# Kernel optimization log

Measured on AMD Instinct MI355X. Metric: run time of the kernel, lower is better.

## Reference

```python
import jax, jax.numpy as jnp
import numpy as np

DIM = 1024
N_HEADS = 16
HEAD_DIM = DIM // N_HEADS


def setup_inputs() -> dict:
    key = jax.random.key(0)
    ks = jax.random.split(key, 5)
    s = 1.0 / np.sqrt(DIM)
    return {
        "x": jax.random.normal(ks[0], (2, 2048, DIM), dtype=jnp.float32),
        "w_qkv": jax.random.normal(ks[1], (DIM, 3 * DIM), dtype=jnp.float32) * s,
        "b_qkv": jnp.zeros((3 * DIM,), dtype=jnp.float32),
        "w_proj": jax.random.normal(ks[2], (DIM, DIM), dtype=jnp.float32) * s,
        "b_proj": jnp.zeros((DIM,), dtype=jnp.float32),
    }


def reference(x, w_qkv, b_qkv, w_proj, b_proj):
    B, T, C = x.shape
    qkv = x @ w_qkv + b_qkv                      # [B,T,3C]
    qkv = qkv.reshape(B, T, 3, N_HEADS, HEAD_DIM)
    q, k, v = qkv[:, :, 0], qkv[:, :, 1], qkv[:, :, 2]  # [B,T,H,D]
    scale = 1.0 / np.sqrt(HEAD_DIM)
    scores = jnp.einsum("bqhd,bkhd->bhqk", q, k) * scale  # [B,H,T,T]
    attn = jax.nn.softmax(scores, axis=-1)
    out = jnp.einsum("bhqk,bkhd->bqhd", attn, v)          # [B,T,H,D]
    out = out.reshape(B, T, C)
    return out @ w_proj + b_proj
```

## Files before the change

kernel.cpp:

```cpp
#include <hip/hip_runtime.h>

typedef unsigned short u16;
typedef unsigned int   u32;
typedef __bf16 bf16x8 __attribute__((ext_vector_type(8)));
typedef float  f32x4  __attribute__((ext_vector_type(4)));
typedef float  f32x16 __attribute__((ext_vector_type(16)));

#define TSEQ 2048
#define NHEAD 16
#define HDIM 64
#define CDIM 1024
#define N3   3072
#define MROWS 4096

__device__ __forceinline__ u16 f2bf(float f) {
    union { float f; u32 u; } v; v.f = f;
    u32 r = v.u + 0x7FFFu + ((v.u >> 16) & 1u);
    return (u16)(r >> 16);
}

__device__ __forceinline__ u32 pkbf(float a, float b) {
#if __has_builtin(__builtin_amdgcn_cvt_pk_bf16_f32)
    typedef __bf16 bf16x2 __attribute__((ext_vector_type(2)));
    bf16x2 t = __builtin_amdgcn_cvt_pk_bf16_f32(a, b);
    union { bf16x2 v; u32 u; } c; c.v = t; return c.u;
#else
    union { float f; u32 u; } ua, ub; ua.f = a; ub.f = b;
    u32 sel = 0x07060302, d;
    asm("v_perm_b32 %0, %1, %2, %3" : "=v"(d) : "v"(ub.u), "v"(ua.u), "v"(sel));
    return d;
#endif
}

__device__ __forceinline__ void gld16(const u16* g, u16* l) {
    __builtin_amdgcn_global_load_lds(
        (const __attribute__((address_space(1))) u32*)g,
        (__attribute__((address_space(3))) u32*)l, 16, 0, 0);
}

__global__ __launch_bounds__(256) void prep_kernel(const float* __restrict__ x,
                                                   const float* __restrict__ wqkv,
                                                   const float* __restrict__ wproj,
                                                   u16* __restrict__ Xb,
                                                   u16* __restrict__ oqkv, u16* __restrict__ oproj) {
    __shared__ float tile[32][33];
    const int bx = blockIdx.x;
    const int tid = threadIdx.x;
    if (bx < 4096) {
        int i = bx * 256 + tid;
        float4 v = reinterpret_cast<const float4*>(x)[i];
        ushort4 o;
        o.x = f2bf(v.x); o.y = f2bf(v.y); o.z = f2bf(v.z); o.w = f2bf(v.w);
        reinterpret_cast<ushort4*>(Xb)[i] = o;
        return;
    }
    int idx = bx - 4096;
    int bnx = idx & 127;
    int k0  = (idx >> 7) * 32;
    const float* in; u16* out; int N, n0;
    if (bnx < 96) { in = wqkv;  out = oqkv;  N = 3072; n0 = bnx * 32; }
    else          { in = wproj; out = oproj; N = 1024; n0 = (bnx - 96) * 32; }
    int tx = tid & 31, ty = tid >> 5;
#pragma unroll
    for (int i = 0; i < 4; i++)
        tile[ty + i * 8][tx] = in[(size_t)(k0 + ty + i * 8) * N + n0 + tx];
    __syncthreads();
#pragma unroll
    for (int i = 0; i < 4; i++)
        out[(size_t)(n0 + ty + i * 8) * 1024 + k0 + tx] = f2bf(tile[tx][ty + i * 8]);
}

__global__ __launch_bounds__(256) void gemm_qkv(const u16* __restrict__ A, const u16* __restrict__ Bt,
                                                const float* __restrict__ bias, u16* __restrict__ Qf,
                                                u16* __restrict__ Kf, u16* __restrict__ Vf) {
    __shared__ __align__(16) u16 Al[128 * 32];
    __shared__ __align__(16) u16 Bl[128 * 32];
    __shared__ __align__(16) u16 Im[16384];
    const int tid  = threadIdx.x;
    const int lane = tid & 63;
    const int wave = tid >> 6;
    const int wm = (wave >> 1) * 64;
    const int wn = (wave & 1) * 64;
    const int row0 = blockIdx.x * 128;
    const int col0 = blockIdx.y * 128;
    const int lr = lane & 15;
    const int lq = lane >> 4;
    const float c2 = 0.125f * 1.44269504088896f;

    f32x4 acc[4][4];
#pragma unroll
    for (int i = 0; i < 4; i++)
#pragma unroll
        for (int j = 0; j < 4; j++) acc[i][j] = f32x4{0.f, 0.f, 0.f, 0.f};

    const int sr = tid >> 2, sc_ = (tid & 3) * 8;

    for (int k0 = 0; k0 < CDIM; k0 += 32) {
#pragma unroll
        for (int s = 0; s < 2; s++) {
            int i = tid + s * 256;
            int r = sr + s * 64;
            gld16(&A[(size_t)(row0 + r) * CDIM + k0 + sc_], &Al[i * 8]);
            gld16(&Bt[(size_t)(col0 + r) * CDIM + k0 + sc_], &Bl[i * 8]);
        }
        __syncthreads();
        bf16x8 af[4], bfr[4];
#pragma unroll
        for (int t = 0; t < 4; t++) {
            af[t]  = *reinterpret_cast<const bf16x8*>(&Al[(wm + t * 16 + lr) * 32 + lq * 8]);
            bfr[t] = *reinterpret_cast<const bf16x8*>(&Bl[(wn + t * 16 + lr) * 32 + lq * 8]);
        }
#pragma unroll
        for (int mt = 0; mt < 4; mt++)
#pragma unroll
            for (int nt = 0; nt < 4; nt++)
                acc[mt][nt] = __builtin_amdgcn_mfma_f32_16x16x32_bf16(af[mt], bfr[nt], acc[mt][nt], 0, 0, 0);
        __syncthreads();
    }

    const int region = col0 >> 10;
    const int h_base = (col0 & 1023) >> 6;
#pragma unroll
    for (int mt = 0; mt < 4; mt++) {
#pragma unroll
        for (int nt = 0; nt < 4; nt++) {
            int n_local = wn + nt * 16 + lr;
            float bv = bias[col0 + n_local];
            int h_local = n_local >> 6;
            int d = n_local & 63;
#pragma unroll
            for (int r = 0; r < 4; r++) {
                int m_local = wm + mt * 16 + lq * 4 + r;
                float v = acc[mt][nt][r] + bv;
                if (region == 0) {
                    int qt_local = m_local >> 5, q31 = m_local & 31;
                    int kc = d >> 4, l5b = (d >> 3) & 1, j = d & 7;
                    int lc = (h_local * 4 + qt_local) * 4 + kc;
                    Im[lc * 512 + (l5b * 32 + q31) * 8 + j] = f2bf(v * c2);
                } else if (region == 1) {
                    int kb_local = m_local >> 6, tr = m_local & 63;
                    int kc = d >> 4, l5b = (d >> 3) & 1, j = d & 7;
                    int nt2 = tr >> 5, p31 = tr & 31;
                    int lc = (h_local * 2 + kb_local) * 8 + kc * 2 + nt2;
                    Im[lc * 512 + (l5b * 32 + p31) * 8 + j] = f2bf(v);
                } else {
                    int kb_local = m_local >> 6, tr = m_local & 63;
                    int cV = tr >> 4, dt2 = d >> 5, p31 = d & 31;
                    int l5b = (tr >> 2) & 1;
                    int j = ((tr >> 3) & 1) * 4 + (tr & 3);
                    int lc = (h_local * 2 + kb_local) * 8 + cV * 2 + dt2;
                    Im[lc * 512 + (l5b * 32 + p31) * 8 + j] = f2bf(v);
                }
            }
        }
    }
    __syncthreads();
    const int bq = row0 >> 11;
    const int qrow0 = row0 & 2047;
#pragma unroll
    for (int s = 0; s < 8; s++) {
        int slot = s * 256 + tid;
        int lc = slot >> 6, li = slot & 63;
        uint4 data = *reinterpret_cast<const uint4*>(&Im[slot * 8]);
        if (region == 0) {
            int h_local = lc >> 4, qt_local = (lc >> 2) & 3, kc = lc & 3;
            size_t off = ((size_t)((bq * 16 + h_base + h_local) * 64 + (qrow0 >> 5) + qt_local) * 4 + kc) * 512
                       + li * 8;
            *reinterpret_cast<uint4*>(Qf + off) = data;
        } else {
            int h_local = lc >> 4, kb_local = (lc >> 3) & 1, cit = lc & 7;
            size_t off = (size_t)((bq * 16 + h_base + h_local) * 32 + (qrow0 >> 6) + kb_local) * 4096
                       + cit * 512 + li * 8;
            *reinterpret_cast<uint4*>((region == 1 ? Kf : Vf) + off) = data;
        }
    }
}

__global__ __launch_bounds__(256) void gemm_proj(const u16* __restrict__ A, const u16* __restrict__ Bt,
                                                 const float* __restrict__ bias, float* __restrict__ C) {
    __shared__ __align__(16) u16 Al[2 * 64 * 32];
    __shared__ __align__(16) u16 Bl[2 * 128 * 32];
    const int tid  = threadIdx.x;
    const int lane = tid & 63;
    const int wave = tid >> 6;
    const int wm = (wave >> 1) * 32;
    const int wn = (wave & 1) * 64;
    const int row0 = blockIdx.x * 64;
    const int col0 = blockIdx.y * 128;
    const int lr = lane & 15;
    const int lq = lane >> 4;

    f32x4 acc[2][4];
#pragma unroll
    for (int i = 0; i < 2; i++)
#pragma unroll
        for (int j = 0; j < 4; j++) acc[i][j] = f32x4{0.f, 0.f, 0.f, 0.f};

    for (int k0 = 0; k0 < CDIM; k0 += 64) {
#pragma unroll
        for (int s = 0; s < 2; s++) {
            int i = tid + s * 256;
            int kk = i >> 8, rr = (i >> 2) & 63, cc = i & 3;
            gld16(&A[(size_t)(row0 + rr) * CDIM + k0 + kk * 32 + cc * 8], &Al[i * 8]);
        }
#pragma unroll
        for (int s = 0; s < 4; s++) {
            int i = tid + s * 256;
            int kk = i >> 9, rr = (i >> 2) & 127, cc = i & 3;
            gld16(&Bt[(size_t)(col0 + rr) * CDIM + k0 + kk * 32 + cc * 8], &Bl[i * 8]);
        }
        __syncthreads();
#pragma unroll
        for (int kk = 0; kk < 2; kk++) {
            bf16x8 af[2], bfr[4];
#pragma unroll
            for (int t = 0; t < 2; t++)
                af[t] = *reinterpret_cast<const bf16x8*>(&Al[kk * 2048 + (wm + t * 16 + lr) * 32 + lq * 8]);
#pragma unroll
            for (int t = 0; t < 4; t++)
                bfr[t] = *reinterpret_cast<const bf16x8*>(&Bl[kk * 4096 + (wn + t * 16 + lr) * 32 + lq * 8]);
#pragma unroll
            for (int mt = 0; mt < 2; mt++)
#pragma unroll
                for (int nt = 0; nt < 4; nt++)
                    acc[mt][nt] = __builtin_amdgcn_mfma_f32_16x16x32_bf16(af[mt], bfr[nt], acc[mt][nt], 0, 0, 0);
        }
        __syncthreads();
    }
#pragma unroll
    for (int mt = 0; mt < 2; mt++) {
#pragma unroll
        for (int nt = 0; nt < 4; nt++) {
            int col = col0 + wn + nt * 16 + lr;
            float bv = bias[col];
#pragma unroll
            for (int r = 0; r < 4; r++) {
                int row = row0 + wm + mt * 16 + lq * 4 + r;
                C[(size_t)row * CDIM + col] = acc[mt][nt][r] + bv;
            }
        }
    }
}

__global__ __launch_bounds__(256, 1) void attn_kernel(const u16* __restrict__ Qf,
                                                      const u16* __restrict__ Kf,
                                                      const u16* __restrict__ Vf,
                                                      u16* __restrict__ AO) {
    const int id = blockIdx.x;
    const int bh = id & 31;
    const int qb = id >> 5;
    const int b = bh >> 4, h = bh & 15;
    const int tid = threadIdx.x, lane = tid & 63, wave = tid >> 6;
    const int l31 = lane & 31, l5 = lane >> 5;
    const int qt0 = qb * 8 + wave * 2;

    bf16x8 qa0[4], qa1[4];
    {
        const u16* qp = Qf + ((size_t)(bh * 64 + qt0) * 4) * 512 + lane * 8;
#pragma unroll
        for (int kc = 0; kc < 4; kc++) {
            qa0[kc] = *reinterpret_cast<const bf16x8*>(qp + kc * 512);
            qa1[kc] = *reinterpret_cast<const bf16x8*>(qp + 2048 + kc * 512);
        }
    }
    f32x16 o00, o01, o10, o11, zc;
#pragma unroll
    for (int i = 0; i < 16; i++) { o00[i] = 0.f; o01[i] = 0.f; o10[i] = 0.f; o11[i] = 0.f; zc[i] = 0.f; }
    float l0 = 0.f, l1 = 0.f;

    const u16* kcur = Kf + (size_t)bh * 32 * 4096 + lane * 8;
    const u16* vcur = Vf + (size_t)bh * 32 * 4096 + lane * 8;

    bf16x8 ka[8];
#pragma unroll
    for (int i = 0; i < 8; i++) ka[i] = *reinterpret_cast<const bf16x8*>(kcur + i * 512);

    for (int kb = 0; kb < 32; kb++) {
        f32x16 st00, st01, st10, st11;
        st00 = __builtin_amdgcn_mfma_f32_32x32x16_bf16(ka[0], qa0[0], zc, 0, 0, 0);
        st01 = __builtin_amdgcn_mfma_f32_32x32x16_bf16(ka[1], qa0[0], zc, 0, 0, 0);
        st10 = __builtin_amdgcn_mfma_f32_32x32x16_bf16(ka[0], qa1[0], zc, 0, 0, 0);
        st11 = __builtin_amdgcn_mfma_f32_32x32x16_bf16(ka[1], qa1[0], zc, 0, 0, 0);
#pragma unroll
        for (int kc = 1; kc < 4; kc++) {
            st00 = __builtin_amdgcn_mfma_f32_32x32x16_bf16(ka[kc * 2],     qa0[kc], st00, 0, 0, 0);
            st01 = __builtin_amdgcn_mfma_f32_32x32x16_bf16(ka[kc * 2 + 1], qa0[kc], st01, 0, 0, 0);
            st10 = __builtin_amdgcn_mfma_f32_32x32x16_bf16(ka[kc * 2],     qa1[kc], st10, 0, 0, 0);
            st11 = __builtin_amdgcn_mfma_f32_32x32x16_bf16(ka[kc * 2 + 1], qa1[kc], st11, 0, 0, 0);
        }
        bf16x8 vfr[8];
#pragma unroll
        for (int i = 0; i < 8; i++) vfr[i] = *reinterpret_cast<const bf16x8*>(vcur + i * 512);
        const u16* knext = kcur + (kb < 31 ? 4096 : 0);
#pragma unroll
        for (int i = 0; i < 8; i++) ka[i] = *reinterpret_cast<const bf16x8*>(knext + i * 512);
        kcur = knext;
        vcur += 4096;
        bf16x8 pa0[4], pa1[4];
        {
            float pe[16];
#pragma unroll
            for (int r = 0; r < 16; r++) { pe[r] = __builtin_amdgcn_exp2f(st00[r]); l0 += pe[r]; }
            union { bf16x8 v; u32 w[4]; } ua, ub;
#pragma unroll
            for (int j = 0; j < 4; j++) { ua.w[j] = pkbf(pe[2 * j], pe[2 * j + 1]); ub.w[j] = pkbf(pe[8 + 2 * j], pe[8 + 2 * j + 1]); }
            pa0[0] = ua.v; pa0[1] = ub.v;
#pragma unroll
            for (int r = 0; r < 16; r++) { pe[r] = __builtin_amdgcn_exp2f(st01[r]); l0 += pe[r]; }
#pragma unroll
            for (int j = 0; j < 4; j++) { ua.w[j] = pkbf(pe[2 * j], pe[2 * j + 1]); ub.w[j] = pkbf(pe[8 + 2 * j], pe[8 + 2 * j + 1]); }
            pa0[2] = ua.v; pa0[3] = ub.v;
#pragma unroll
            for (int r = 0; r < 16; r++) { pe[r] = __builtin_amdgcn_exp2f(st10[r]); l1 += pe[r]; }
#pragma unroll
            for (int j = 0; j < 4; j++) { ua.w[j] = pkbf(pe[2 * j], pe[2 * j + 1]); ub.w[j] = pkbf(pe[8 + 2 * j], pe[8 + 2 * j + 1]); }
            pa1[0] = ua.v; pa1[1] = ub.v;
#pragma unroll
            for (int r = 0; r < 16; r++) { pe[r] = __builtin_amdgcn_exp2f(st11[r]); l1 += pe[r]; }
#pragma unroll
            for (int j = 0; j < 4; j++) { ua.w[j] = pkbf(pe[2 * j], pe[2 * j + 1]); ub.w[j] = pkbf(pe[8 + 2 * j], pe[8 + 2 * j + 1]); }
            pa1[2] = ua.v; pa1[3] = ub.v;
        }
#pragma unroll
        for (int c = 0; c < 4; c++) {
            o00 = __builtin_amdgcn_mfma_f32_32x32x16_bf16(pa0[c], vfr[c * 2],     o00, 0, 0, 0);
            o01 = __builtin_amdgcn_mfma_f32_32x32x16_bf16(pa0[c], vfr[c * 2 + 1], o01, 0, 0, 0);
            o10 = __builtin_amdgcn_mfma_f32_32x32x16_bf16(pa1[c], vfr[c * 2],     o10, 0, 0, 0);
            o11 = __builtin_amdgcn_mfma_f32_32x32x16_bf16(pa1[c], vfr[c * 2 + 1], o11, 0, 0, 0);
        }
    }
    {
        float l = l0;
        l += __shfl_xor(l, 32);
        float linv = 1.0f / l;
        int q0 = qt0 * 32;
#pragma unroll
        for (int reg = 0; reg < 16; reg++) {
            int qrow = (reg & 3) + 8 * (reg >> 2) + 4 * l5;
            float li = __shfl(linv, qrow);
            AO[(size_t)(b * TSEQ + q0 + qrow) * CDIM + h * 64 + l31]      = f2bf(o00[reg] * li);
            AO[(size_t)(b * TSEQ + q0 + qrow) * CDIM + h * 64 + 32 + l31] = f2bf(o01[reg] * li);
        }
    }
    {
        float l = l1;
        l += __shfl_xor(l, 32);
        float linv = 1.0f / l;
        int q0 = (qt0 + 1) * 32;
#pragma unroll
        for (int reg = 0; reg < 16; reg++) {
            int qrow = (reg & 3) + 8 * (reg >> 2) + 4 * l5;
            float li = __shfl(linv, qrow);
            AO[(size_t)(b * TSEQ + q0 + qrow) * CDIM + h * 64 + l31]      = f2bf(o10[reg] * li);
            AO[(size_t)(b * TSEQ + q0 + qrow) * CDIM + h * 64 + 32 + l31] = f2bf(o11[reg] * li);
        }
    }
}

extern "C" void kernel_launch(void* const* d_in, const int* in_sizes, int n_in,
                              void* d_out, int out_size, void* d_ws, size_t ws_size,
                              hipStream_t stream) {
    const float* x      = (const float*)d_in[0];
    const float* w_qkv  = (const float*)d_in[1];
    const float* b_qkv  = (const float*)d_in[2];
    const float* w_proj = (const float*)d_in[3];
    const float* b_proj = (const float*)d_in[4];
    float* out = (float*)d_out;

    u16* ws     = (u16*)d_ws;
    u16* Xb     = ws;
    u16* Wqkvt  = Xb + 4194304;
    u16* Wprojt = Wqkvt + 3145728;
    u16* Qf     = Wprojt + 1048576;
    u16* Kf     = Qf + 4194304;
    u16* Vf     = Kf + 4194304;
    u16* AO     = Vf + 4194304;

    prep_kernel<<<8192, 256, 0, stream>>>(x, w_qkv, w_proj, Xb, Wqkvt, Wprojt);
    gemm_qkv<<<dim3(32, 24), 256, 0, stream>>>(Xb, Wqkvt, b_qkv, Qf, Kf, Vf);
    attn_kernel<<<256, 256, 0, stream>>>(Qf, Kf, Vf, AO);
    gemm_proj<<<dim3(64, 8), 256, 0, stream>>>(AO, Wprojt, b_proj, out);
}
```

Measured before the change: 173.6 us.

## Halve per-wave query tiles in attention, double grid, raise occupancy, add setprio

Each wave in the attention kernel now handles one 32-row query tile instead of two, and the grid grows from 256 to 512 blocks with launch bounds allowing two blocks per CU. This cuts register pressure and spreads work over more CUs (256 blocks on a 256-CU part left little latency hiding). The V loads move ahead of the QK MFMAs, s_setprio brackets the MFMA sections, and the row-sum accumulator is split four ways to shorten the dependency chain. In exchange, every K/V tile is loaded twice as often from global memory or cache, since each K/V fragment now feeds only one query tile per wave.

```diff
diff --git a/kernel.cpp b/kernel.cpp
--- a/kernel.cpp
+++ b/kernel.cpp
@@ -242,7 +242,7 @@
     }
 }
 
-__global__ __launch_bounds__(256, 1) void attn_kernel(const u16* __restrict__ Qf,
+__global__ __launch_bounds__(256, 2) void attn_kernel(const u16* __restrict__ Qf,
                                                       const u16* __restrict__ Kf,
                                                       const u16* __restrict__ Vf,
                                                       u16* __restrict__ AO) {
@@ -252,21 +252,21 @@
     const int b = bh >> 4, h = bh & 15;
     const int tid = threadIdx.x, lane = tid & 63, wave = tid >> 6;
     const int l31 = lane & 31, l5 = lane >> 5;
-    const int qt0 = qb * 8 + wave * 2;
-
-    bf16x8 qa0[4], qa1[4];
+    const int qt = qb * 4 + wave;
+
+    bf16x8 qa[4];
     {
-        const u16* qp = Qf + ((size_t)(bh * 64 + qt0) * 4) * 512 + lane * 8;
-#pragma unroll
-        for (int kc = 0; kc < 4; kc++) {
-            qa0[kc] = *reinterpret_cast<const bf16x8*>(qp + kc * 512);
-            qa1[kc] = *reinterpret_cast<const bf16x8*>(qp + 2048 + kc * 512);
-        }
-    }
-    f32x16 o00, o01, o10, o11, zc;
-#pragma unroll
-    for (int i = 0; i < 16; i++) { o00[i] = 0.f; o01[i] = 0.f; o10[i] = 0.f; o11[i] = 0.f; zc[i] = 0.f; }
-    float l0 = 0.f, l1 = 0.f;
+        const u16* qp = Qf + ((size_t)(bh * 64 + qt) * 4) * 512 + lane * 8;
+#pragma unroll
+        for (int kc = 0; kc < 4; kc++)
+            qa[kc] = *reinterpret_cast<const bf16x8*>(qp + kc * 512);
+    }
+    f32x16 o0, o1, zc;
+#pragma unroll
+    for (int i = 0; i < 16; i++) { o0[i] = 0.f; o1[i] = 0.f; zc[i] = 0.f; }
+    float lacc[4];
+#pragma unroll
+    for (int i = 0; i < 4; i++) lacc[i] = 0.f;
 
     const u16* kcur = Kf + (size_t)bh * 32 * 4096 + lane * 8;
     const u16* vcur = Vf + (size_t)bh * 32 * 4096 + lane * 8;
@@ -276,83 +276,58 @@
     for (int i = 0; i < 8; i++) ka[i] = *reinterpret_cast<const bf16x8*>(kcur + i * 512);
 
     for (int kb = 0; kb < 32; kb++) {
-        f32x16 st00, st01, st10, st11;
-        st00 = __builtin_amdgcn_mfma_f32_32x32x16_bf16(ka[0], qa0[0], zc, 0, 0, 0);
-        st01 = __builtin_amdgcn_mfma_f32_32x32x16_bf16(ka[1], qa0[0], zc, 0, 0, 0);
-        st10 = __builtin_amdgcn_mfma_f32_32x32x16_bf16(ka[0], qa1[0], zc, 0, 0, 0);
-        st11 = __builtin_amdgcn_mfma_f32_32x32x16_bf16(ka[1], qa1[0], zc, 0, 0, 0);
+        bf16x8 vfr[8];
+#pragma unroll
+        for (int i = 0; i < 8; i++) vfr[i] = *reinterpret_cast<const bf16x8*>(vcur + i * 512);
+        f32x16 st0, st1;
+        __builtin_amdgcn_s_setprio(1);
+        st0 = __builtin_amdgcn_mfma_f32_32x32x16_bf16(ka[0], qa[0], zc, 0, 0, 0);
+        st1 = __builtin_amdgcn_mfma_f32_32x32x16_bf16(ka[1], qa[0], zc, 0, 0, 0);
 #pragma unroll
         for (int kc = 1; kc < 4; kc++) {
-            st00 = __builtin_amdgcn_mfma_f32_32x32x16_bf16(ka[kc * 2],     qa0[kc], st00, 0, 0, 0);
-            st01 = __builtin_amdgcn_mfma_f32_32x32x16_bf16(ka[kc * 2 + 1], qa0[kc], st01, 0, 0, 0);
-            st10 = __builtin_amdgcn_mfma_f32_32x32x16_bf16(ka[kc * 2],     qa1[kc], st10, 0, 0, 0);
-            st11 = __builtin_amdgcn_mfma_f32_32x32x16_bf16(ka[kc * 2 + 1], qa1[kc], st11, 0, 0, 0);
-        }
-        bf16x8 vfr[8];
-#pragma unroll
-        for (int i = 0; i < 8; i++) vfr[i] = *reinterpret_cast<const bf16x8*>(vcur + i * 512);
+            st0 = __builtin_amdgcn_mfma_f32_32x32x16_bf16(ka[kc * 2],     qa[kc], st0, 0, 0, 0);
+            st1 = __builtin_amdgcn_mfma_f32_32x32x16_bf16(ka[kc * 2 + 1], qa[kc], st1, 0, 0, 0);
+        }
+        __builtin_amdgcn_s_setprio(0);
         const u16* knext = kcur + (kb < 31 ? 4096 : 0);
 #pragma unroll
         for (int i = 0; i < 8; i++) ka[i] = *reinterpret_cast<const bf16x8*>(knext + i * 512);
         kcur = knext;
         vcur += 4096;
-        bf16x8 pa0[4], pa1[4];
+        bf16x8 pa[4];
         {
             float pe[16];
-#pragma unroll
-            for (int r = 0; r < 16; r++) { pe[r] = __builtin_amdgcn_exp2f(st00[r]); l0 += pe[r]; }
             union { bf16x8 v; u32 w[4]; } ua, ub;
 #pragma unroll
+            for (int r = 0; r < 16; r++) { pe[r] = __builtin_amdgcn_exp2f(st0[r]); lacc[r & 3] += pe[r]; }
+#pragma unroll
             for (int j = 0; j < 4; j++) { ua.w[j] = pkbf(pe[2 * j], pe[2 * j + 1]); ub.w[j] = pkbf(pe[8 + 2 * j], pe[8 + 2 * j + 1]); }
-            pa0[0] = ua.v; pa0[1] = ub.v;
-#pragma unroll
-            for (int r = 0; r < 16; r++) { pe[r] = __builtin_amdgcn_exp2f(st01[r]); l0 += pe[r]; }
+            pa[0] = ua.v; pa[1] = ub.v;
+#pragma unroll
+            for (int r = 0; r < 16; r++) { pe[r] = __builtin_amdgcn_exp2f(st1[r]); lacc[r & 3] += pe[r]; }
 #pragma unroll
             for (int j = 0; j < 4; j++) { ua.w[j] = pkbf(pe[2 * j], pe[2 * j + 1]); ub.w[j] = pkbf(pe[8 + 2 * j], pe[8 + 2 * j + 1]); }
-            pa0[2] = ua.v; pa0[3] = ub.v;
-#pragma unroll
-            for (int r = 0; r < 16; r++) { pe[r] = __builtin_amdgcn_exp2f(st10[r]); l1 += pe[r]; }
-#pragma unroll
-            for (int j = 0; j < 4; j++) { ua.w[j] = pkbf(pe[2 * j], pe[2 * j + 1]); ub.w[j] = pkbf(pe[8 + 2 * j], pe[8 + 2 * j + 1]); }
-            pa1[0] = ua.v; pa1[1] = ub.v;
-#pragma unroll
-            for (int r = 0; r < 16; r++) { pe[r] = __builtin_amdgcn_exp2f(st11[r]); l1 += pe[r]; }
-#pragma unroll
-            for (int j = 0; j < 4; j++) { ua.w[j] = pkbf(pe[2 * j], pe[2 * j + 1]); ub.w[j] = pkbf(pe[8 + 2 * j], pe[8 + 2 * j + 1]); }
-            pa1[2] = ua.v; pa1[3] = ub.v;
-        }
+            pa[2] = ua.v; pa[3] = ub.v;
+        }
+        __builtin_amdgcn_s_setprio(1);
 #pragma unroll
         for (int c = 0; c < 4; c++) {
-            o00 = __builtin_amdgcn_mfma_f32_32x32x16_bf16(pa0[c], vfr[c * 2],     o00, 0, 0, 0);
-            o01 = __builtin_amdgcn_mfma_f32_32x32x16_bf16(pa0[c], vfr[c * 2 + 1], o01, 0, 0, 0);
-            o10 = __builtin_amdgcn_mfma_f32_32x32x16_bf16(pa1[c], vfr[c * 2],     o10, 0, 0, 0);
-            o11 = __builtin_amdgcn_mfma_f32_32x32x16_bf16(pa1[c], vfr[c * 2 + 1], o11, 0, 0, 0);
-        }
+            o0 = __builtin_amdgcn_mfma_f32_32x32x16_bf16(pa[c], vfr[c * 2],     o0, 0, 0, 0);
+            o1 = __builtin_amdgcn_mfma_f32_32x32x16_bf16(pa[c], vfr[c * 2 + 1], o1, 0, 0, 0);
+        }
+        __builtin_amdgcn_s_setprio(0);
     }
     {
-        float l = l0;
+        float l = (lacc[0] + lacc[1]) + (lacc[2] + lacc[3]);
         l += __shfl_xor(l, 32);
         float linv = 1.0f / l;
-        int q0 = qt0 * 32;
+        int q0 = qt * 32;
 #pragma unroll
         for (int reg = 0; reg < 16; reg++) {
             int qrow = (reg & 3) + 8 * (reg >> 2) + 4 * l5;
             float li = __shfl(linv, qrow);
-            AO[(size_t)(b * TSEQ + q0 + qrow) * CDIM + h * 64 + l31]      = f2bf(o00[reg] * li);
-            AO[(size_t)(b * TSEQ + q0 + qrow) * CDIM + h * 64 + 32 + l31] = f2bf(o01[reg] * li);
-        }
-    }
-    {
-        float l = l1;
-        l += __shfl_xor(l, 32);
-        float linv = 1.0f / l;
-        int q0 = (qt0 + 1) * 32;
-#pragma unroll
-        for (int reg = 0; reg < 16; reg++) {
-            int qrow = (reg & 3) + 8 * (reg >> 2) + 4 * l5;
-            float li = __shfl(linv, qrow);
-            AO[(size_t)(b * TSEQ + q0 + qrow) * CDIM + h * 64 + l31]      = f2bf(o10[reg] * li);
-            AO[(size_t)(b * TSEQ + q0 + qrow) * CDIM + h * 64 + 32 + l31] = f2bf(o11[reg] * li);
+            AO[(size_t)(b * TSEQ + q0 + qrow) * CDIM + h * 64 + l31]      = f2bf(o0[reg] * li);
+            AO[(size_t)(b * TSEQ + q0 + qrow) * CDIM + h * 64 + 32 + l31] = f2bf(o1[reg] * li);
         }
     }
 }
@@ -378,6 +353,6 @@
 
     prep_kernel<<<8192, 256, 0, stream>>>(x, w_qkv, w_proj, Xb, Wqkvt, Wprojt);
     gemm_qkv<<<dim3(32, 24), 256, 0, stream>>>(Xb, Wqkvt, b_qkv, Qf, Kf, Vf);
-    attn_kernel<<<256, 256, 0, stream>>>(Qf, Kf, Vf, AO);
+    attn_kernel<<<512, 256, 0, stream>>>(Qf, Kf, Vf, AO);
     gemm_proj<<<dim3(64, 8), 256, 0, stream>>>(AO, Wprojt, b_proj, out);
 }
```

After: 181.1 us. 4.3% more time.

## Software-pipeline attention loop: overlap next QK^T MFMAs with current softmax

Applied to the files above, without the earlier changes.

Restructures the attention inner loop so the QK^T scores for the next key block are computed while the exp/pack softmax of the current block runs, using ping-pong score registers and a 2x-unrolled loop. K fragments are prefetched two blocks ahead. The row-sum accumulator is split into four partial sums to shorten the serial add chain. This aims to hide MFMA latency behind VALU work, at the cost of more live accumulator registers and possible spills. The final iteration computes one redundant QK^T block on the clamped last K tile.

```diff
diff --git a/kernel.cpp b/kernel.cpp
--- a/kernel.cpp
+++ b/kernel.cpp
@@ -242,6 +242,65 @@
     }
 }
 
+#define SUBITER(KB, SP00, SP01, SP10, SP11, SN00, SN01, SN10, SN11)                                  \
+  {                                                                                                  \
+    bf16x8 vfr[8];                                                                                   \
+    _Pragma("unroll") for (int i = 0; i < 8; i++)                                                    \
+        vfr[i] = *reinterpret_cast<const bf16x8*>(vcur + i * 512);                                   \
+    vcur += 4096;                                                                                    \
+                                          \
+    SN00 = __builtin_amdgcn_mfma_f32_32x32x16_bf16(ka[0], qa0[0], zc, 0, 0, 0);                      \
+    SN01 = __builtin_amdgcn_mfma_f32_32x32x16_bf16(ka[1], qa0[0], zc, 0, 0, 0);                      \
+    SN10 = __builtin_amdgcn_mfma_f32_32x32x16_bf16(ka[0], qa1[0], zc, 0, 0, 0);                      \
+    SN11 = __builtin_amdgcn_mfma_f32_32x32x16_bf16(ka[1], qa1[0], zc, 0, 0, 0);                      \
+    _Pragma("unroll") for (int kc = 1; kc < 4; kc++) {                                               \
+      SN00 = __builtin_amdgcn_mfma_f32_32x32x16_bf16(ka[kc * 2],     qa0[kc], SN00, 0, 0, 0);        \
+      SN01 = __builtin_amdgcn_mfma_f32_32x32x16_bf16(ka[kc * 2 + 1], qa0[kc], SN01, 0, 0, 0);        \
+      SN10 = __builtin_amdgcn_mfma_f32_32x32x16_bf16(ka[kc * 2],     qa1[kc], SN10, 0, 0, 0);        \
+      SN11 = __builtin_amdgcn_mfma_f32_32x32x16_bf16(ka[kc * 2 + 1], qa1[kc], SN11, 0, 0, 0);        \
+    }                                                                                                \
+                                                \
+    bf16x8 pa0[4], pa1[4];                                                                           \
+    {                                                                                                \
+      float pe[16];                                                                                  \
+      union { bf16x8 v; u32 w[4]; } ua, ub;                                                          \
+      _Pragma("unroll") for (int r = 0; r < 16; r++) {                                               \
+        pe[r] = __builtin_amdgcn_exp2f(SP00[r]); la0[r & 3] += pe[r]; }                              \
+      _Pragma("unroll") for (int j = 0; j < 4; j++) {                                                \
+        ua.w[j] = pkbf(pe[2 * j], pe[2 * j + 1]); ub.w[j] = pkbf(pe[8 + 2 * j], pe[8 + 2 * j + 1]); }\
+      pa0[0] = ua.v; pa0[1] = ub.v;                                                                  \
+      _Pragma("unroll") for (int r = 0; r < 16; r++) {                                               \
+        pe[r] = __builtin_amdgcn_exp2f(SP01[r]); la0[r & 3] += pe[r]; }                              \
+      _Pragma("unroll") for (int j = 0; j < 4; j++) {                                                \
+        ua.w[j] = pkbf(pe[2 * j], pe[2 * j + 1]); ub.w[j] = pkbf(pe[8 + 2 * j], pe[8 + 2 * j + 1]); }\
+      pa0[2] = ua.v; pa0[3] = ub.v;                                                                  \
+      _Pragma("unroll") for (int r = 0; r < 16; r++) {                                               \
+        pe[r] = __builtin_amdgcn_exp2f(SP10[r]); la1[r & 3] += pe[r]; }                              \
+      _Pragma("unroll") for (int j = 0; j < 4; j++) {                                                \
+        ua.w[j] = pkbf(pe[2 * j], pe[2 * j + 1]); ub.w[j] = pkbf(pe[8 + 2 * j], pe[8 + 2 * j + 1]); }\
+      pa1[0] = ua.v; pa1[1] = ub.v;                                                                  \
+      _Pragma("unroll") for (int r = 0; r < 16; r++) {                                               \
+        pe[r] = __builtin_amdgcn_exp2f(SP11[r]); la1[r & 3] += pe[r]; }                              \
+      _Pragma("unroll") for (int j = 0; j < 4; j++) {                                                \
+        ua.w[j] = pkbf(pe[2 * j], pe[2 * j + 1]); ub.w[j] = pkbf(pe[8 + 2 * j], pe[8 + 2 * j + 1]); }\
+      pa1[2] = ua.v; pa1[3] = ub.v;                                                                  \
+    }                                                                                                \
+                                          \
+    {                                                                                                \
+      int knext = (KB) + 2; if (knext > 31) knext = 31;                                              \
+      const u16* kp = kbase + (size_t)knext * 4096;                                                  \
+      _Pragma("unroll") for (int i = 0; i < 8; i++)                                                  \
+        ka[i] = *reinterpret_cast<const bf16x8*>(kp + i * 512);                                      \
+    }                                                                                                \
+                                                                                       \
+    _Pragma("unroll") for (int c = 0; c < 4; c++) {                                                  \
+      o00 = __builtin_amdgcn_mfma_f32_32x32x16_bf16(pa0[c], vfr[c * 2],     o00, 0, 0, 0);           \
+      o01 = __builtin_amdgcn_mfma_f32_32x32x16_bf16(pa0[c], vfr[c * 2 + 1], o01, 0, 0, 0);           \
+      o10 = __builtin_amdgcn_mfma_f32_32x32x16_bf16(pa1[c], vfr[c * 2],     o10, 0, 0, 0);           \
+      o11 = __builtin_amdgcn_mfma_f32_32x32x16_bf16(pa1[c], vfr[c * 2 + 1], o11, 0, 0, 0);           \
+    }                                                                                                \
+  }
+
 __global__ __launch_bounds__(256, 1) void attn_kernel(const u16* __restrict__ Qf,
                                                       const u16* __restrict__ Kf,
                                                       const u16* __restrict__ Vf,
@@ -266,71 +325,40 @@
     f32x16 o00, o01, o10, o11, zc;
 #pragma unroll
     for (int i = 0; i < 16; i++) { o00[i] = 0.f; o01[i] = 0.f; o10[i] = 0.f; o11[i] = 0.f; zc[i] = 0.f; }
-    float l0 = 0.f, l1 = 0.f;
-
-    const u16* kcur = Kf + (size_t)bh * 32 * 4096 + lane * 8;
-    const u16* vcur = Vf + (size_t)bh * 32 * 4096 + lane * 8;
+    float la0[4], la1[4];
+#pragma unroll
+    for (int i = 0; i < 4; i++) { la0[i] = 0.f; la1[i] = 0.f; }
+
+    const u16* kbase = Kf + (size_t)bh * 32 * 4096 + lane * 8;
+    const u16* vcur  = Vf + (size_t)bh * 32 * 4096 + lane * 8;
 
     bf16x8 ka[8];
 #pragma unroll
-    for (int i = 0; i < 8; i++) ka[i] = *reinterpret_cast<const bf16x8*>(kcur + i * 512);
-
-    for (int kb = 0; kb < 32; kb++) {
-        f32x16 st00, st01, st10, st11;
-        st00 = __builtin_amdgcn_mfma_f32_32x32x16_bf16(ka[0], qa0[0], zc, 0, 0, 0);
-        st01 = __builtin_amdgcn_mfma_f32_32x32x16_bf16(ka[1], qa0[0], zc, 0, 0, 0);
-        st10 = __builtin_amdgcn_mfma_f32_32x32x16_bf16(ka[0], qa1[0], zc, 0, 0, 0);
-        st11 = __builtin_amdgcn_mfma_f32_32x32x16_bf16(ka[1], qa1[0], zc, 0, 0, 0);
-#pragma unroll
-        for (int kc = 1; kc < 4; kc++) {
-            st00 = __builtin_amdgcn_mfma_f32_32x32x16_bf16(ka[kc * 2],     qa0[kc], st00, 0, 0, 0);
-            st01 = __builtin_amdgcn_mfma_f32_32x32x16_bf16(ka[kc * 2 + 1], qa0[kc], st01, 0, 0, 0);
-            st10 = __builtin_amdgcn_mfma_f32_32x32x16_bf16(ka[kc * 2],     qa1[kc], st10, 0, 0, 0);
-            st11 = __builtin_amdgcn_mfma_f32_32x32x16_bf16(ka[kc * 2 + 1], qa1[kc], st11, 0, 0, 0);
-        }
-        bf16x8 vfr[8];
-#pragma unroll
-        for (int i = 0; i < 8; i++) vfr[i] = *reinterpret_cast<const bf16x8*>(vcur + i * 512);
-        const u16* knext = kcur + (kb < 31 ? 4096 : 0);
-#pragma unroll
-        for (int i = 0; i < 8; i++) ka[i] = *reinterpret_cast<const bf16x8*>(knext + i * 512);
-        kcur = knext;
-        vcur += 4096;
-        bf16x8 pa0[4], pa1[4];
-        {
-            float pe[16];
-#pragma unroll
-            for (int r = 0; r < 16; r++) { pe[r] = __builtin_amdgcn_exp2f(st00[r]); l0 += pe[r]; }
-            union { bf16x8 v; u32 w[4]; } ua, ub;
-#pragma unroll
-            for (int j = 0; j < 4; j++) { ua.w[j] = pkbf(pe[2 * j], pe[2 * j + 1]); ub.w[j] = pkbf(pe[8 + 2 * j], pe[8 + 2 * j + 1]); }
-            pa0[0] = ua.v; pa0[1] = ub.v;
-#pragma unroll
-            for (int r = 0; r < 16; r++) { pe[r] = __builtin_amdgcn_exp2f(st01[r]); l0 += pe[r]; }
-#pragma unroll
-            for (int j = 0; j < 4; j++) { ua.w[j] = pkbf(pe[2 * j], pe[2 * j + 1]); ub.w[j] = pkbf(pe[8 + 2 * j], pe[8 + 2 * j + 1]); }
-            pa0[2] = ua.v; pa0[3] = ub.v;
-#pragma unroll
-            for (int r = 0; r < 16; r++) { pe[r] = __builtin_amdgcn_exp2f(st10[r]); l1 += pe[r]; }
-#pragma unroll
-            for (int j = 0; j < 4; j++) { ua.w[j] = pkbf(pe[2 * j], pe[2 * j + 1]); ub.w[j] = pkbf(pe[8 + 2 * j], pe[8 + 2 * j + 1]); }
-            pa1[0] = ua.v; pa1[1] = ub.v;
-#pragma unroll
-            for (int r = 0; r < 16; r++) { pe[r] = __builtin_amdgcn_exp2f(st11[r]); l1 += pe[r]; }
-#pragma unroll
-            for (int j = 0; j < 4; j++) { ua.w[j] = pkbf(pe[2 * j], pe[2 * j + 1]); ub.w[j] = pkbf(pe[8 + 2 * j], pe[8 + 2 * j + 1]); }
-            pa1[2] = ua.v; pa1[3] = ub.v;
-        }
-#pragma unroll
-        for (int c = 0; c < 4; c++) {
-            o00 = __builtin_amdgcn_mfma_f32_32x32x16_bf16(pa0[c], vfr[c * 2],     o00, 0, 0, 0);
-            o01 = __builtin_amdgcn_mfma_f32_32x32x16_bf16(pa0[c], vfr[c * 2 + 1], o01, 0, 0, 0);
-            o10 = __builtin_amdgcn_mfma_f32_32x32x16_bf16(pa1[c], vfr[c * 2],     o10, 0, 0, 0);
-            o11 = __builtin_amdgcn_mfma_f32_32x32x16_bf16(pa1[c], vfr[c * 2 + 1], o11, 0, 0, 0);
-        }
-    }
+    for (int i = 0; i < 8; i++) ka[i] = *reinterpret_cast<const bf16x8*>(kbase + i * 512);
+
+    f32x16 sA0, sA1, sA2, sA3, sB0, sB1, sB2, sB3;
+    sA0 = __builtin_amdgcn_mfma_f32_32x32x16_bf16(ka[0], qa0[0], zc, 0, 0, 0);
+    sA1 = __builtin_amdgcn_mfma_f32_32x32x16_bf16(ka[1], qa0[0], zc, 0, 0, 0);
+    sA2 = __builtin_amdgcn_mfma_f32_32x32x16_bf16(ka[0], qa1[0], zc, 0, 0, 0);
+    sA3 = __builtin_amdgcn_mfma_f32_32x32x16_bf16(ka[1], qa1[0], zc, 0, 0, 0);
+#pragma unroll
+    for (int kc = 1; kc < 4; kc++) {
+        sA0 = __builtin_amdgcn_mfma_f32_32x32x16_bf16(ka[kc * 2],     qa0[kc], sA0, 0, 0, 0);
+        sA1 = __builtin_amdgcn_mfma_f32_32x32x16_bf16(ka[kc * 2 + 1], qa0[kc], sA1, 0, 0, 0);
+        sA2 = __builtin_amdgcn_mfma_f32_32x32x16_bf16(ka[kc * 2],     qa1[kc], sA2, 0, 0, 0);
+        sA3 = __builtin_amdgcn_mfma_f32_32x32x16_bf16(ka[kc * 2 + 1], qa1[kc], sA3, 0, 0, 0);
+    }
+#pragma unroll
+    for (int i = 0; i < 8; i++) ka[i] = *reinterpret_cast<const bf16x8*>(kbase + 4096 + i * 512);
+
+    for (int kb2 = 0; kb2 < 16; kb2++) {
+        int kb = kb2 * 2;
+        SUBITER(kb,     sA0, sA1, sA2, sA3, sB0, sB1, sB2, sB3);
+        SUBITER(kb + 1, sB0, sB1, sB2, sB3, sA0, sA1, sA2, sA3);
+    }
+
     {
-        float l = l0;
+        float l = (la0[0] + la0[1]) + (la0[2] + la0[3]);
         l += __shfl_xor(l, 32);
         float linv = 1.0f / l;
         int q0 = qt0 * 32;
@@ -343,7 +371,7 @@
         }
     }
     {
-        float l = l1;
+        float l = (la1[0] + la1[1]) + (la1[2] + la1[3]);
         l += __shfl_xor(l, 32);
         float linv = 1.0f / l;
         int q0 = (qt0 + 1) * 32;
```

New measurement: 172.6 us. About the same (-0.6%).

## Split attention KV range across two wave halves and merge partial outputs in LDS

Applied to the files above, without the earlier changes.

The attention kernel now launches 512 threads per block, with two groups of four waves each handling half of the key/value sequence for the same query tiles. The second half writes its partial output and row sums to shared memory, and the first half adds them before normalising and storing. Softmax has no max subtraction, so the partials combine by plain addition. The change also moves the V loads earlier, wraps the MFMA sections in s_setprio, and splits the row-sum accumulation across four registers. The aim is to double the waves per CU and hide latency with 256 blocks on a 256-CU part, at the cost of LDS traffic, a block-wide sync and more register pressure.

```diff
diff --git a/kernel.cpp b/kernel.cpp
--- a/kernel.cpp
+++ b/kernel.cpp
@@ -242,17 +242,21 @@
     }
 }
 
-__global__ __launch_bounds__(256, 1) void attn_kernel(const u16* __restrict__ Qf,
+__global__ __launch_bounds__(512, 2) void attn_kernel(const u16* __restrict__ Qf,
                                                       const u16* __restrict__ Kf,
                                                       const u16* __restrict__ Vf,
                                                       u16* __restrict__ AO) {
+    __shared__ __align__(16) float Ol[4][16][64][4];
+    __shared__ float Ll[4][64][2];
     const int id = blockIdx.x;
     const int bh = id & 31;
-    const int qb = id >> 5;
+    const int qc = id >> 5;
     const int b = bh >> 4, h = bh & 15;
     const int tid = threadIdx.x, lane = tid & 63, wave = tid >> 6;
+    const int wp   = wave & 3;
+    const int half = wave >> 2;
     const int l31 = lane & 31, l5 = lane >> 5;
-    const int qt0 = qb * 8 + wave * 2;
+    const int qt0 = qc * 8 + wp * 2;
 
     bf16x8 qa0[4], qa1[4];
     {
@@ -266,17 +270,23 @@
     f32x16 o00, o01, o10, o11, zc;
 #pragma unroll
     for (int i = 0; i < 16; i++) { o00[i] = 0.f; o01[i] = 0.f; o10[i] = 0.f; o11[i] = 0.f; zc[i] = 0.f; }
-    float l0 = 0.f, l1 = 0.f;
-
-    const u16* kcur = Kf + (size_t)bh * 32 * 4096 + lane * 8;
-    const u16* vcur = Vf + (size_t)bh * 32 * 4096 + lane * 8;
+    float la0[4], la1[4];
+#pragma unroll
+    for (int i = 0; i < 4; i++) { la0[i] = 0.f; la1[i] = 0.f; }
+
+    const u16* kcur = Kf + ((size_t)bh * 32 + half * 16) * 4096 + lane * 8;
+    const u16* vcur = Vf + ((size_t)bh * 32 + half * 16) * 4096 + lane * 8;
 
     bf16x8 ka[8];
 #pragma unroll
     for (int i = 0; i < 8; i++) ka[i] = *reinterpret_cast<const bf16x8*>(kcur + i * 512);
 
-    for (int kb = 0; kb < 32; kb++) {
+    for (int kb = 0; kb < 16; kb++) {
+        bf16x8 vfr[8];
+#pragma unroll
+        for (int i = 0; i < 8; i++) vfr[i] = *reinterpret_cast<const bf16x8*>(vcur + i * 512);
         f32x16 st00, st01, st10, st11;
+        __builtin_amdgcn_s_setprio(1);
         st00 = __builtin_amdgcn_mfma_f32_32x32x16_bf16(ka[0], qa0[0], zc, 0, 0, 0);
         st01 = __builtin_amdgcn_mfma_f32_32x32x16_bf16(ka[1], qa0[0], zc, 0, 0, 0);
         st10 = __builtin_amdgcn_mfma_f32_32x32x16_bf16(ka[0], qa1[0], zc, 0, 0, 0);
@@ -288,10 +298,8 @@
             st10 = __builtin_amdgcn_mfma_f32_32x32x16_bf16(ka[kc * 2],     qa1[kc], st10, 0, 0, 0);
             st11 = __builtin_amdgcn_mfma_f32_32x32x16_bf16(ka[kc * 2 + 1], qa1[kc], st11, 0, 0, 0);
         }
-        bf16x8 vfr[8];
-#pragma unroll
-        for (int i = 0; i < 8; i++) vfr[i] = *reinterpret_cast<const bf16x8*>(vcur + i * 512);
-        const u16* knext = kcur + (kb < 31 ? 4096 : 0);
+        __builtin_amdgcn_s_setprio(0);
+        const u16* knext = kcur + (kb < 15 ? 4096 : 0);
 #pragma unroll
         for (int i = 0; i < 8; i++) ka[i] = *reinterpret_cast<const bf16x8*>(knext + i * 512);
         kcur = knext;
@@ -299,28 +307,29 @@
         bf16x8 pa0[4], pa1[4];
         {
             float pe[16];
-#pragma unroll
-            for (int r = 0; r < 16; r++) { pe[r] = __builtin_amdgcn_exp2f(st00[r]); l0 += pe[r]; }
             union { bf16x8 v; u32 w[4]; } ua, ub;
+#pragma unroll
+            for (int r = 0; r < 16; r++) { pe[r] = __builtin_amdgcn_exp2f(st00[r]); la0[r & 3] += pe[r]; }
 #pragma unroll
             for (int j = 0; j < 4; j++) { ua.w[j] = pkbf(pe[2 * j], pe[2 * j + 1]); ub.w[j] = pkbf(pe[8 + 2 * j], pe[8 + 2 * j + 1]); }
             pa0[0] = ua.v; pa0[1] = ub.v;
 #pragma unroll
-            for (int r = 0; r < 16; r++) { pe[r] = __builtin_amdgcn_exp2f(st01[r]); l0 += pe[r]; }
+            for (int r = 0; r < 16; r++) { pe[r] = __builtin_amdgcn_exp2f(st01[r]); la0[r & 3] += pe[r]; }
 #pragma unroll
             for (int j = 0; j < 4; j++) { ua.w[j] = pkbf(pe[2 * j], pe[2 * j + 1]); ub.w[j] = pkbf(pe[8 + 2 * j], pe[8 + 2 * j + 1]); }
             pa0[2] = ua.v; pa0[3] = ub.v;
 #pragma unroll
-            for (int r = 0; r < 16; r++) { pe[r] = __builtin_amdgcn_exp2f(st10[r]); l1 += pe[r]; }
+            for (int r = 0; r < 16; r++) { pe[r] = __builtin_amdgcn_exp2f(st10[r]); la1[r & 3] += pe[r]; }
 #pragma unroll
             for (int j = 0; j < 4; j++) { ua.w[j] = pkbf(pe[2 * j], pe[2 * j + 1]); ub.w[j] = pkbf(pe[8 + 2 * j], pe[8 + 2 * j + 1]); }
             pa1[0] = ua.v; pa1[1] = ub.v;
 #pragma unroll
-            for (int r = 0; r < 16; r++) { pe[r] = __builtin_amdgcn_exp2f(st11[r]); l1 += pe[r]; }
+            for (int r = 0; r < 16; r++) { pe[r] = __builtin_amdgcn_exp2f(st11[r]); la1[r & 3] += pe[r]; }
 #pragma unroll
             for (int j = 0; j < 4; j++) { ua.w[j] = pkbf(pe[2 * j], pe[2 * j + 1]); ub.w[j] = pkbf(pe[8 + 2 * j], pe[8 + 2 * j + 1]); }
             pa1[2] = ua.v; pa1[3] = ub.v;
         }
+        __builtin_amdgcn_s_setprio(1);
 #pragma unroll
         for (int c = 0; c < 4; c++) {
             o00 = __builtin_amdgcn_mfma_f32_32x32x16_bf16(pa0[c], vfr[c * 2],     o00, 0, 0, 0);
@@ -328,7 +337,41 @@
             o10 = __builtin_amdgcn_mfma_f32_32x32x16_bf16(pa1[c], vfr[c * 2],     o10, 0, 0, 0);
             o11 = __builtin_amdgcn_mfma_f32_32x32x16_bf16(pa1[c], vfr[c * 2 + 1], o11, 0, 0, 0);
         }
-    }
+        __builtin_amdgcn_s_setprio(0);
+    }
+
+    float l0 = (la0[0] + la0[1]) + (la0[2] + la0[3]);
+    float l1 = (la1[0] + la1[1]) + (la1[2] + la1[3]);
+    if (half == 1) {
+#pragma unroll
+        for (int g = 0; g < 4; g++) {
+            *reinterpret_cast<f32x4*>(&Ol[wp][g][lane][0])      = f32x4{o00[4*g], o00[4*g+1], o00[4*g+2], o00[4*g+3]};
+            *reinterpret_cast<f32x4*>(&Ol[wp][g + 4][lane][0])  = f32x4{o01[4*g], o01[4*g+1], o01[4*g+2], o01[4*g+3]};
+            *reinterpret_cast<f32x4*>(&Ol[wp][g + 8][lane][0])  = f32x4{o10[4*g], o10[4*g+1], o10[4*g+2], o10[4*g+3]};
+            *reinterpret_cast<f32x4*>(&Ol[wp][g + 12][lane][0]) = f32x4{o11[4*g], o11[4*g+1], o11[4*g+2], o11[4*g+3]};
+        }
+        Ll[wp][lane][0] = l0;
+        Ll[wp][lane][1] = l1;
+    }
+    __syncthreads();
+    if (half == 1) return;
+    l0 += Ll[wp][lane][0];
+    l1 += Ll[wp][lane][1];
+#pragma unroll
+    for (int g = 0; g < 4; g++) {
+        f32x4 a0 = *reinterpret_cast<const f32x4*>(&Ol[wp][g][lane][0]);
+        f32x4 a1 = *reinterpret_cast<const f32x4*>(&Ol[wp][g + 4][lane][0]);
+        f32x4 a2 = *reinterpret_cast<const f32x4*>(&Ol[wp][g + 8][lane][0]);
+        f32x4 a3 = *reinterpret_cast<const f32x4*>(&Ol[wp][g + 12][lane][0]);
+#pragma unroll
+        for (int j = 0; j < 4; j++) {
+            o00[4*g + j] += a0[j];
+            o01[4*g + j] += a1[j];
+            o10[4*g + j] += a2[j];
+            o11[4*g + j] += a3[j];
+        }
+    }
+
     {
         float l = l0;
         l += __shfl_xor(l, 32);
@@ -378,6 +421,6 @@
 
     prep_kernel<<<8192, 256, 0, stream>>>(x, w_qkv, w_proj, Xb, Wqkvt, Wprojt);
     gemm_qkv<<<dim3(32, 24), 256, 0, stream>>>(Xb, Wqkvt, b_qkv, Qf, Kf, Vf);
-    attn_kernel<<<256, 256, 0, stream>>>(Qf, Kf, Vf, AO);
+    attn_kernel<<<256, 512, 0, stream>>>(Qf, Kf, Vf, AO);
     gemm_proj<<<dim3(64, 8), 256, 0, stream>>>(AO, Wprojt, b_proj, out);
 }
```

Result: slower. 187.6 us (+8.1%).
